# Kernel tuning notes

Hardware: AMD Instinct MI355X
Metric: run time of the kernel (lower is better)

Reference implementation:

```python
import jax, jax.numpy as jnp
import numpy as np

EMBED = 768
HEADS = 12
HEAD_DIM = EMBED // HEADS
HIDDEN = int(EMBED * 4.0)
EPS = 1e-5


def setup_inputs() -> dict:
    key = jax.random.key(0)
    ks = jax.random.split(key, 12)
    s = 0.02
    return {
        "x": jax.random.normal(ks[0], (8, 1024, EMBED), dtype=jnp.float32),
        # norm1 / norm2 (LayerNorm affine params)
        "g1": jnp.ones((EMBED,), jnp.float32),
        "b1": jnp.zeros((EMBED,), jnp.float32),
        "g2": jnp.ones((EMBED,), jnp.float32),
        "b2": jnp.zeros((EMBED,), jnp.float32),
        # attention weights (stored [in, out]; qkv_bias=False)
        "w_qkv": jax.random.normal(ks[1], (EMBED, 3 * EMBED), jnp.float32) * s,
        "w_proj": jax.random.normal(ks[2], (EMBED, EMBED), jnp.float32) * s,
        "b_proj": jnp.zeros((EMBED,), jnp.float32),
        # MLP weights
        "w_fc1": jax.random.normal(ks[3], (EMBED, HIDDEN), jnp.float32) * s,
        "b_fc1": jnp.zeros((HIDDEN,), jnp.float32),
        "w_fc2": jax.random.normal(ks[4], (HIDDEN, EMBED), jnp.float32) * s,
        "b_fc2": jnp.zeros((EMBED,), jnp.float32),
    }


def _layernorm(x, g, b):
    mu = jnp.mean(x, axis=-1, keepdims=True)
    var = jnp.var(x, axis=-1, keepdims=True)
    return (x - mu) * jax.lax.rsqrt(var + EPS) * g + b


def reference(x, g1, b1, g2, b2, w_qkv, w_proj, b_proj, w_fc1, b_fc1, w_fc2, b_fc2):
    B, N, C = x.shape
    scaling = HEAD_DIM ** (-0.5)

    # --- attention branch ---
    h = _layernorm(x, g1, b1)
    qkv = (h @ w_qkv).reshape(B, N, 3, HEADS, HEAD_DIM)
    q, k, v = qkv[:, :, 0], qkv[:, :, 1], qkv[:, :, 2]  # [B, N, H, D]
    attn = jnp.einsum("bnhd,bmhd->bhnm", q, k) * scaling  # full NxN scores
    attn = jax.nn.softmax(attn, axis=-1)
    out = jnp.einsum("bhnm,bmhd->bnhd", attn, v).reshape(B, N, C)
    out = out @ w_proj + b_proj
    x = x + out

    # --- MLP branch ---
    h = _layernorm(x, g2, b2)
    h = jax.nn.gelu(h @ w_fc1 + b_fc1, approximate=False)
    h = h @ w_fc2 + b_fc2
    return x + h
```

## Files before the change

kernel.cpp:

```cpp
#include <hip/hip_runtime.h>
#include <hip/hip_bf16.h>
#include <math.h>

#define EMBED 768
#define HEADS 12
#define HEAD_DIM 64
#define HIDDEN 3072
#define SEQ 1024
#define BATCH 8
#define TOKENS (SEQ*BATCH)

typedef unsigned short u16;
typedef __attribute__((ext_vector_type(8))) short bf16x8;
typedef __attribute__((ext_vector_type(4))) float floatx4;
typedef __attribute__((ext_vector_type(4))) u16 u16x4;
typedef __attribute__((ext_vector_type(2))) u16 u16x2;

__device__ __forceinline__ u16 f2bf(float f){
    union { float f; unsigned u; } v; v.f = f;
    unsigned r = v.u + 0x7fffu + ((v.u >> 16) & 1u);
    return (u16)(r >> 16);
}

__device__ __forceinline__ void gload16(const void* g, void* l){
    __builtin_amdgcn_global_load_lds((const __attribute__((address_space(1))) void*)g,
                                     (__attribute__((address_space(3))) void*)l, 16, 0, 0);
}

__device__ __forceinline__ float gelu_fast(float x){
    float t = 1.5957691216f * (x + 0.044715f * x * x * x);
    return x / (1.0f + __expf(-t));
}

__global__ void transpose_cast(const float* __restrict__ W, u16* __restrict__ Wt, int K, int N){
    __shared__ float tile[32][33];
    int n0 = blockIdx.x * 32, k0 = blockIdx.y * 32;
    int tx = threadIdx.x, ty = threadIdx.y;
    #pragma unroll
    for(int i=0;i<32;i+=8) tile[ty+i][tx] = W[(size_t)(k0+ty+i)*N + n0+tx];
    __syncthreads();
    int tid = ty*32 + tx;
    int kp = (tid & 15)*2, nn = tid >> 4;
    #pragma unroll
    for(int p=0;p<2;p++){
        int n = nn + p*16;
        u16x2 w2;
        w2.x = f2bf(tile[kp  ][n]);
        w2.y = f2bf(tile[kp+1][n]);
        *(u16x2*)(Wt + (size_t)(n0+n)*K + k0 + kp) = w2;
    }
}

__global__ __launch_bounds__(256) void ln_kernel(const float* __restrict__ x, const float* __restrict__ g,
                                                 const float* __restrict__ b, u16* __restrict__ out){
    int row  = blockIdx.x * 4 + (threadIdx.x >> 6);
    int lane = threadIdx.x & 63;
    const float4* xr = (const float4*)(x + (size_t)row * EMBED);
    float4 v[3];
    float s = 0.f;
    #pragma unroll
    for(int i=0;i<3;i++){
        v[i] = xr[i*64 + lane];
        s += v[i].x + v[i].y + v[i].z + v[i].w;
    }
    #pragma unroll
    for(int o=32;o>0;o>>=1) s += __shfl_xor(s, o);
    float mu = s * (1.0f/EMBED);
    float s2 = 0.f;
    #pragma unroll
    for(int i=0;i<3;i++){
        float dx = v[i].x-mu, dy = v[i].y-mu, dz = v[i].z-mu, dw = v[i].w-mu;
        s2 += dx*dx + dy*dy + dz*dz + dw*dw;
    }
    #pragma unroll
    for(int o=32;o>0;o>>=1) s2 += __shfl_xor(s2, o);
    float rstd = rsqrtf(s2*(1.0f/EMBED) + 1e-5f);
    u16* orow = out + (size_t)row * EMBED;
    const float4* g4 = (const float4*)g;
    const float4* b4 = (const float4*)b;
    #pragma unroll
    for(int i=0;i<3;i++){
        int c4 = i*64 + lane;
        float4 gv = g4[c4], bv = b4[c4];
        u16x4 pk;
        pk.x = f2bf((v[i].x-mu)*rstd*gv.x + bv.x);
        pk.y = f2bf((v[i].y-mu)*rstd*gv.y + bv.y);
        pk.z = f2bf((v[i].z-mu)*rstd*gv.z + bv.z);
        pk.w = f2bf((v[i].w-mu)*rstd*gv.w + bv.w);
        *(u16x4*)(orow + c4*4) = pk;
    }
}

template<int EPI, int BM>
__global__ __launch_bounds__(256) void gemm_bt(const u16* __restrict__ A, const u16* __restrict__ Bt,
        void* __restrict__ Cout, const float* __restrict__ bias, const float* __restrict__ res,
        u16* __restrict__ vt, int M, int N, int K, int ldc){
    constexpr int MF = BM/32;
    __shared__ __align__(16) u16 As[BM*64];
    __shared__ __align__(16) u16 Bs[128*64];
    int tid  = threadIdx.x;
    int wave = tid >> 6, lane = tid & 63;
    int quad = lane >> 4, lm = lane & 15;
    int m0 = blockIdx.y * BM, n0 = blockIdx.x * 128;
    int wm = (wave & 1) * (BM/2);
    int wn = (wave >> 1) * 64;

    floatx4 acc[MF][4];
    #pragma unroll
    for(int i=0;i<MF;i++)
        #pragma unroll
        for(int j=0;j<4;j++) acc[i][j] = (floatx4){0.f,0.f,0.f,0.f};

    int srow = tid >> 3;
    int scol = ((tid & 7) ^ (srow & 7)) * 8;
    const u16* aP[MF];
    const u16* bP[4];
    #pragma unroll
    for(int p=0;p<MF;p++) aP[p] = A  + (size_t)(m0 + p*32 + srow) * K + scol;
    #pragma unroll
    for(int p=0;p<4;p++)  bP[p] = Bt + (size_t)(n0 + p*32 + srow) * K + scol;

    for(int k0=0; k0<K; k0+=64){
        __syncthreads();
        #pragma unroll
        for(int p=0;p<MF;p++) gload16(aP[p] + k0, As + p*2048 + tid*8);
        #pragma unroll
        for(int p=0;p<4;p++)  gload16(bP[p] + k0, Bs + p*2048 + tid*8);
        __syncthreads();
        #pragma unroll
        for(int ks=0;ks<2;ks++){
            int slotoff = (((ks*4+quad) ^ (lm&7)) << 3);
            bf16x8 af[MF], bfr[4];
            #pragma unroll
            for(int i=0;i<MF;i++)
                af[i]  = *(const bf16x8*)(As + (wm + i*16 + lm)*64 + slotoff);
            #pragma unroll
            for(int i=0;i<4;i++)
                bfr[i] = *(const bf16x8*)(Bs + (wn + i*16 + lm)*64 + slotoff);
            #pragma unroll
            for(int mf=0;mf<MF;mf++)
                #pragma unroll
                for(int nf=0;nf<4;nf++)
                    acc[mf][nf] = __builtin_amdgcn_mfma_f32_16x16x32_bf16(af[mf], bfr[nf], acc[mf][nf], 0, 0, 0);
        }
    }

    if(EPI == 3 && n0 >= 1536){
        #pragma unroll
        for(int nf=0;nf<4;nf++){
            int col = n0 + wn + nf*16 + lm;
            int hh = (col - 1536) >> 6;
            int d  = col & 63;
            #pragma unroll
            for(int mf=0;mf<MF;mf++){
                int row0 = m0 + wm + mf*16 + quad*4;
                int bb  = row0 >> 10;
                int key = row0 & 1023;
                u16x4 pk;
                #pragma unroll
                for(int r=0;r<4;r++) pk[r] = f2bf(acc[mf][nf][r]);
                *(u16x4*)(vt + ((size_t)(bb*HEADS+hh)*64 + d)*SEQ + key) = pk;
            }
        }
        return;
    }

    #pragma unroll
    for(int nf=0;nf<4;nf++){
        int col = n0 + wn + nf*16 + lm;
        float bv = bias ? bias[col] : 0.f;
        #pragma unroll
        for(int mf=0;mf<MF;mf++){
            int row0 = m0 + wm + mf*16 + quad*4;
            #pragma unroll
            for(int r=0;r<4;r++){
                float v = acc[mf][nf][r] + bv;
                size_t idx = (size_t)(row0 + r) * ldc + col;
                if(EPI == 1){
                    v = gelu_fast(v);
                    ((u16*)Cout)[idx] = f2bf(v);
                } else if(EPI == 2){
                    ((float*)Cout)[idx] = v + res[idx];
                } else {
                    ((u16*)Cout)[idx] = f2bf(v);
                }
            }
        }
    }
}

__global__ __launch_bounds__(256) void attn_kernel(const u16* __restrict__ qk, const u16* __restrict__ vt,
                                                   u16* __restrict__ out){
    int qt = blockIdx.x, h = blockIdx.y, b = blockIdx.z;
    int tid = threadIdx.x;
    int wave = tid >> 6, lane = tid & 63;
    int quad = lane >> 4, lm = lane & 15;

    __shared__ __align__(16) u16 Ks[64*64];
    __shared__ __align__(16) u16 Vs[64*64];
    __shared__ __align__(16) u16 P[4*32*64];

    const u16* qbase = qk + (size_t)b * SEQ * 1536;
    const u16* vbase = vt + (size_t)(b*HEADS + h) * 64 * SEQ;
    u16* Pw = P + wave*2048;

    int q0 = qt*128 + wave*32;
    bf16x8 qf[2][2];
    #pragma unroll
    for(int qi=0;qi<2;qi++){
        const u16* qp = qbase + (size_t)(q0 + qi*16 + lm)*1536 + h*64;
        qf[qi][0] = *(const bf16x8*)(qp + quad*8);
        qf[qi][1] = *(const bf16x8*)(qp + 32 + quad*8);
    }

    float l_i[2] = {0.f, 0.f};
    floatx4 o_acc[2][4];
    #pragma unroll
    for(int qi=0;qi<2;qi++)
        #pragma unroll
        for(int nf=0;nf<4;nf++) o_acc[qi][nf] = (floatx4){0.f,0.f,0.f,0.f};

    int sr = lane >> 3;
    int sp = lane & 7;
    const float C = 0.18033688011112186f;

    for(int kt=0; kt<16; kt++){
        __syncthreads();
        #pragma unroll
        for(int i=0;i<2;i++){
            int rr = wave*16 + i*8 + sr;
            int sw = (sp ^ (rr & 7)) * 8;
            gload16(qbase + (size_t)(kt*64 + rr)*1536 + 768 + h*64 + sw,
                    Ks + (wave*16 + i*8)*64 + lane*8);
            gload16(vbase + (size_t)rr*SEQ + kt*64 + sw,
                    Vs + (wave*16 + i*8)*64 + lane*8);
        }
        __syncthreads();

        floatx4 s[4][2];
        #pragma unroll
        for(int kf=0;kf<4;kf++){
            int krow = kf*16 + lm;
            bf16x8 k0 = *(const bf16x8*)(Ks + krow*64 + ((quad     ^ (lm&7))*8));
            bf16x8 k1 = *(const bf16x8*)(Ks + krow*64 + (((4+quad) ^ (lm&7))*8));
            #pragma unroll
            for(int qi=0;qi<2;qi++){
                floatx4 t = (floatx4){0.f,0.f,0.f,0.f};
                t = __builtin_amdgcn_mfma_f32_16x16x32_bf16(k0, qf[qi][0], t, 0, 0, 0);
                t = __builtin_amdgcn_mfma_f32_16x16x32_bf16(k1, qf[qi][1], t, 0, 0, 0);
                s[kf][qi] = t;
            }
        }

        #pragma unroll
        for(int qi=0;qi<2;qi++){
            float part = 0.f;
            #pragma unroll
            for(int kf=0;kf<4;kf++){
                #pragma unroll
                for(int r=0;r<4;r++){
                    float e = exp2f(s[kf][qi][r]*C);
                    s[kf][qi][r] = e;
                    part += e;
                }
            }
            part += __shfl_xor(part, 16);
            part += __shfl_xor(part, 32);
            l_i[qi] += part;
            #pragma unroll
            for(int kf=0;kf<4;kf++){
                u16x4 pk;
                #pragma unroll
                for(int r=0;r<4;r++) pk[r] = f2bf(s[kf][qi][r]);
                int c  = kf*4 + quad;
                int cp = c ^ (2*(lm & 7));
                *(u16x4*)(Pw + (qi*16 + lm)*64 + cp*4) = pk;
            }
        }

        #pragma unroll
        for(int ks=0;ks<2;ks++){
            bf16x8 vf[4];
            #pragma unroll
            for(int nf=0;nf<4;nf++)
                vf[nf] = *(const bf16x8*)(Vs + (nf*16+lm)*64 + (((ks*4+quad) ^ (lm&7))*8));
            #pragma unroll
            for(int qi=0;qi<2;qi++){
                int cr = (ks*8 + 2*quad) ^ (2*(lm & 7));
                bf16x8 pa = *(const bf16x8*)(Pw + (qi*16 + lm)*64 + cr*4);
                #pragma unroll
                for(int nf=0;nf<4;nf++)
                    o_acc[qi][nf] = __builtin_amdgcn_mfma_f32_16x16x32_bf16(pa, vf[nf], o_acc[qi][nf], 0, 0, 0);
            }
        }
    }

    #pragma unroll
    for(int qi=0;qi<2;qi++){
        float rl[4];
        #pragma unroll
        for(int r=0;r<4;r++) rl[r] = 1.0f / __shfl(l_i[qi], quad*4 + r);
        int token = b*SEQ + qt*128 + wave*32 + qi*16 + quad*4;
        #pragma unroll
        for(int nf=0;nf<4;nf++){
            #pragma unroll
            for(int r=0;r<4;r++){
                out[(size_t)(token + r)*EMBED + h*64 + nf*16 + lm] = f2bf(o_acc[qi][nf][r] * rl[r]);
            }
        }
    }
}

extern "C" void kernel_launch(void* const* d_in, const int* in_sizes, int n_in,
                              void* d_out, int out_size, void* d_ws, size_t ws_size,
                              hipStream_t stream) {
    const float* x      = (const float*)d_in[0];
    const float* g1     = (const float*)d_in[1];
    const float* b1     = (const float*)d_in[2];
    const float* g2     = (const float*)d_in[3];
    const float* b2     = (const float*)d_in[4];
    const float* w_qkv  = (const float*)d_in[5];
    const float* w_proj = (const float*)d_in[6];
    const float* b_proj = (const float*)d_in[7];
    const float* w_fc1  = (const float*)d_in[8];
    const float* b_fc1  = (const float*)d_in[9];
    const float* w_fc2  = (const float*)d_in[10];
    const float* b_fc2  = (const float*)d_in[11];
    float* out = (float*)d_out;

    char* ws = (char*)d_ws;
    u16*   wqkv_t  = (u16*)  (ws + 0);
    u16*   wproj_t = (u16*)  (ws + 3538944);
    u16*   wfc1_t  = (u16*)  (ws + 4718592);
    u16*   wfc2_t  = (u16*)  (ws + 9437184);
    float* x1      = (float*)(ws + 14155776);
    u16*   hbuf    = (u16*)  (ws + 39321600);
    u16*   qkbuf   = (u16*)  (ws + 51904512);
    u16*   vtbuf   = (u16*)  (ws + 77070336);
    u16*   attn_o  = (u16*)  (ws + 89653248);
    u16*   fc1_o   = qkbuf;
    u16*   h2      = hbuf;

    dim3 tb(32, 8);
    transpose_cast<<<dim3(2304/32,  768/32), tb, 0, stream>>>(w_qkv,  wqkv_t,  768, 2304);
    transpose_cast<<<dim3( 768/32,  768/32), tb, 0, stream>>>(w_proj, wproj_t, 768,  768);
    transpose_cast<<<dim3(3072/32,  768/32), tb, 0, stream>>>(w_fc1,  wfc1_t,  768, 3072);
    transpose_cast<<<dim3( 768/32, 3072/32), tb, 0, stream>>>(w_fc2,  wfc2_t, 3072,  768);

    ln_kernel<<<TOKENS/4, 256, 0, stream>>>(x, g1, b1, hbuf);

    gemm_bt<3,128><<<dim3(2304/128, TOKENS/128), 256, 0, stream>>>(hbuf, wqkv_t, qkbuf, nullptr, nullptr, vtbuf, TOKENS, 2304, 768, 1536);

    attn_kernel<<<dim3(8, HEADS, BATCH), 256, 0, stream>>>(qkbuf, vtbuf, attn_o);

    gemm_bt<2,64><<<dim3( 768/128, TOKENS/64), 256, 0, stream>>>(attn_o, wproj_t, x1, b_proj, x, nullptr, TOKENS, 768, 768, 768);

    ln_kernel<<<TOKENS/4, 256, 0, stream>>>(x1, g2, b2, h2);

    gemm_bt<1,128><<<dim3(3072/128, TOKENS/128), 256, 0, stream>>>(h2, wfc1_t, fc1_o, b_fc1, nullptr, nullptr, TOKENS, 3072, 768, 3072);

    gemm_bt<2,64><<<dim3( 768/128, TOKENS/64), 256, 0, stream>>>(fc1_o, wfc2_t, out, b_fc2, x1, nullptr, TOKENS, 768, 3072, 768);
}
```

Measured before the change: 380.6 us.

## Double-buffer LDS tiles in GEMM and attention, merge weight transpose launches

The GEMM and attention kernels now keep two LDS buffers. They issue global-to-LDS loads for the next K/V or K-tile before computing on the current one, so there is one barrier per iteration instead of two and load latency can overlap with MFMA work. The four weight transpose-cast launches are merged into a single launch that dispatches on block index. The extra buffers double LDS use, which may lower occupancy, and the prefetch relies on the barrier at the end of each iteration to stay correct.

```diff
diff --git a/kernel.cpp b/kernel.cpp
--- a/kernel.cpp
+++ b/kernel.cpp
@@ -32,9 +32,19 @@
     return x / (1.0f + __expf(-t));
 }
 
-__global__ void transpose_cast(const float* __restrict__ W, u16* __restrict__ Wt, int K, int N){
+__global__ void transpose_cast_all(const float* __restrict__ w0, const float* __restrict__ w1,
+                                   const float* __restrict__ w2, const float* __restrict__ w3,
+                                   u16* __restrict__ o0, u16* __restrict__ o1,
+                                   u16* __restrict__ o2, u16* __restrict__ o3){
+    int bb = blockIdx.x;
+    const float* W; u16* Wt; int K, N, bx, by;
+    if(bb < 1728)      { int l = bb;        W=w0; Wt=o0; K=768;  N=2304; bx=l%72; by=l/72; }
+    else if(bb < 2304) { int l = bb-1728;   W=w1; Wt=o1; K=768;  N=768;  bx=l%24; by=l/24; }
+    else if(bb < 4608) { int l = bb-2304;   W=w2; Wt=o2; K=768;  N=3072; bx=l%96; by=l/96; }
+    else               { int l = bb-4608;   W=w3; Wt=o3; K=3072; N=768;  bx=l%24; by=l/24; }
+
     __shared__ float tile[32][33];
-    int n0 = blockIdx.x * 32, k0 = blockIdx.y * 32;
+    int n0 = bx * 32, k0 = by * 32;
     int tx = threadIdx.x, ty = threadIdx.y;
     #pragma unroll
     for(int i=0;i<32;i+=8) tile[ty+i][tx] = W[(size_t)(k0+ty+i)*N + n0+tx];
@@ -44,10 +54,10 @@
     #pragma unroll
     for(int p=0;p<2;p++){
         int n = nn + p*16;
-        u16x2 w2;
-        w2.x = f2bf(tile[kp  ][n]);
-        w2.y = f2bf(tile[kp+1][n]);
-        *(u16x2*)(Wt + (size_t)(n0+n)*K + k0 + kp) = w2;
+        u16x2 w2v;
+        w2v.x = f2bf(tile[kp  ][n]);
+        w2v.y = f2bf(tile[kp+1][n]);
+        *(u16x2*)(Wt + (size_t)(n0+n)*K + k0 + kp) = w2v;
     }
 }
 
@@ -95,9 +105,11 @@
 __global__ __launch_bounds__(256) void gemm_bt(const u16* __restrict__ A, const u16* __restrict__ Bt,
         void* __restrict__ Cout, const float* __restrict__ bias, const float* __restrict__ res,
         u16* __restrict__ vt, int M, int N, int K, int ldc){
-    constexpr int MF = BM/32;
-    __shared__ __align__(16) u16 As[BM*64];
-    __shared__ __align__(16) u16 Bs[128*64];
+    constexpr int MF  = BM/32;
+    constexpr int ASZ = BM*64;
+    constexpr int BSZ = 128*64;
+    __shared__ __align__(16) u16 As[2*ASZ];
+    __shared__ __align__(16) u16 Bs[2*BSZ];
     int tid  = threadIdx.x;
     int wave = tid >> 6, lane = tid & 63;
     int quad = lane >> 4, lm = lane & 15;
@@ -120,29 +132,41 @@
     #pragma unroll
     for(int p=0;p<4;p++)  bP[p] = Bt + (size_t)(n0 + p*32 + srow) * K + scol;
 
+    #pragma unroll
+    for(int p=0;p<MF;p++) gload16(aP[p], As + p*2048 + tid*8);
+    #pragma unroll
+    for(int p=0;p<4;p++)  gload16(bP[p], Bs + p*2048 + tid*8);
+    __syncthreads();
+
+    int cur = 0;
     for(int k0=0; k0<K; k0+=64){
-        __syncthreads();
-        #pragma unroll
-        for(int p=0;p<MF;p++) gload16(aP[p] + k0, As + p*2048 + tid*8);
-        #pragma unroll
-        for(int p=0;p<4;p++)  gload16(bP[p] + k0, Bs + p*2048 + tid*8);
-        __syncthreads();
+        int nxt = cur ^ 1;
+        if(k0 + 64 < K){
+            #pragma unroll
+            for(int p=0;p<MF;p++) gload16(aP[p] + k0 + 64, As + nxt*ASZ + p*2048 + tid*8);
+            #pragma unroll
+            for(int p=0;p<4;p++)  gload16(bP[p] + k0 + 64, Bs + nxt*BSZ + p*2048 + tid*8);
+        }
+        const u16* Asb = As + cur*ASZ;
+        const u16* Bsb = Bs + cur*BSZ;
         #pragma unroll
         for(int ks=0;ks<2;ks++){
             int slotoff = (((ks*4+quad) ^ (lm&7)) << 3);
             bf16x8 af[MF], bfr[4];
             #pragma unroll
             for(int i=0;i<MF;i++)
-                af[i]  = *(const bf16x8*)(As + (wm + i*16 + lm)*64 + slotoff);
+                af[i]  = *(const bf16x8*)(Asb + (wm + i*16 + lm)*64 + slotoff);
             #pragma unroll
             for(int i=0;i<4;i++)
-                bfr[i] = *(const bf16x8*)(Bs + (wn + i*16 + lm)*64 + slotoff);
+                bfr[i] = *(const bf16x8*)(Bsb + (wn + i*16 + lm)*64 + slotoff);
             #pragma unroll
             for(int mf=0;mf<MF;mf++)
                 #pragma unroll
                 for(int nf=0;nf<4;nf++)
                     acc[mf][nf] = __builtin_amdgcn_mfma_f32_16x16x32_bf16(af[mf], bfr[nf], acc[mf][nf], 0, 0, 0);
         }
+        if(k0 + 64 < K) __syncthreads();
+        cur = nxt;
     }
 
     if(EPI == 3 && n0 >= 1536){
@@ -196,8 +220,8 @@
     int wave = tid >> 6, lane = tid & 63;
     int quad = lane >> 4, lm = lane & 15;
 
-    __shared__ __align__(16) u16 Ks[64*64];
-    __shared__ __align__(16) u16 Vs[64*64];
+    __shared__ __align__(16) u16 Ks[2*64*64];
+    __shared__ __align__(16) u16 Vs[2*64*64];
     __shared__ __align__(16) u16 P[4*32*64];
 
     const u16* qbase = qk + (size_t)b * SEQ * 1536;
@@ -224,25 +248,33 @@
     int sp = lane & 7;
     const float C = 0.18033688011112186f;
 
-    for(int kt=0; kt<16; kt++){
-        __syncthreads();
+    auto stage = [&](int kt, int buf){
         #pragma unroll
         for(int i=0;i<2;i++){
             int rr = wave*16 + i*8 + sr;
             int sw = (sp ^ (rr & 7)) * 8;
             gload16(qbase + (size_t)(kt*64 + rr)*1536 + 768 + h*64 + sw,
-                    Ks + (wave*16 + i*8)*64 + lane*8);
+                    Ks + buf*4096 + (wave*16 + i*8)*64 + lane*8);
             gload16(vbase + (size_t)rr*SEQ + kt*64 + sw,
-                    Vs + (wave*16 + i*8)*64 + lane*8);
-        }
-        __syncthreads();
+                    Vs + buf*4096 + (wave*16 + i*8)*64 + lane*8);
+        }
+    };
+
+    stage(0, 0);
+    __syncthreads();
+
+    int cur = 0;
+    for(int kt=0; kt<16; kt++){
+        if(kt < 15) stage(kt+1, cur^1);
+        const u16* Ksb = Ks + cur*4096;
+        const u16* Vsb = Vs + cur*4096;
 
         floatx4 s[4][2];
         #pragma unroll
         for(int kf=0;kf<4;kf++){
             int krow = kf*16 + lm;
-            bf16x8 k0 = *(const bf16x8*)(Ks + krow*64 + ((quad     ^ (lm&7))*8));
-            bf16x8 k1 = *(const bf16x8*)(Ks + krow*64 + (((4+quad) ^ (lm&7))*8));
+            bf16x8 k0 = *(const bf16x8*)(Ksb + krow*64 + ((quad     ^ (lm&7))*8));
+            bf16x8 k1 = *(const bf16x8*)(Ksb + krow*64 + (((4+quad) ^ (lm&7))*8));
             #pragma unroll
             for(int qi=0;qi<2;qi++){
                 floatx4 t = (floatx4){0.f,0.f,0.f,0.f};
@@ -283,7 +315,7 @@
             bf16x8 vf[4];
             #pragma unroll
             for(int nf=0;nf<4;nf++)
-                vf[nf] = *(const bf16x8*)(Vs + (nf*16+lm)*64 + (((ks*4+quad) ^ (lm&7))*8));
+                vf[nf] = *(const bf16x8*)(Vsb + (nf*16+lm)*64 + (((ks*4+quad) ^ (lm&7))*8));
             #pragma unroll
             for(int qi=0;qi<2;qi++){
                 int cr = (ks*8 + 2*quad) ^ (2*(lm & 7));
@@ -293,6 +325,8 @@
                     o_acc[qi][nf] = __builtin_amdgcn_mfma_f32_16x16x32_bf16(pa, vf[nf], o_acc[qi][nf], 0, 0, 0);
             }
         }
+        if(kt < 15) __syncthreads();
+        cur ^= 1;
     }
 
     #pragma unroll
@@ -341,11 +375,8 @@
     u16*   fc1_o   = qkbuf;
     u16*   h2      = hbuf;
 
-    dim3 tb(32, 8);
-    transpose_cast<<<dim3(2304/32,  768/32), tb, 0, stream>>>(w_qkv,  wqkv_t,  768, 2304);
-    transpose_cast<<<dim3( 768/32,  768/32), tb, 0, stream>>>(w_proj, wproj_t, 768,  768);
-    transpose_cast<<<dim3(3072/32,  768/32), tb, 0, stream>>>(w_fc1,  wfc1_t,  768, 3072);
-    transpose_cast<<<dim3( 768/32, 3072/32), tb, 0, stream>>>(w_fc2,  wfc2_t, 3072,  768);
+    transpose_cast_all<<<6912, dim3(32,8), 0, stream>>>(w_qkv, w_proj, w_fc1, w_fc2,
+                                                        wqkv_t, wproj_t, wfc1_t, wfc2_t);
 
     ln_kernel<<<TOKENS/4, 256, 0, stream>>>(x, g1, b1, hbuf);
 
```

New measurement: 381.2 us. Within noise of the previous version (+0.2%).
